# Performance work log

Measured on AMD Instinct MI355X. Metric: run time of the kernel, lower is better.

The kernel has to match this reference:

```python
import jax, jax.numpy as jnp
import numpy as np

V, H, B, T, L = 10000, 1024, 64, 32, 2  # vocab, hidden, batch, target_len, num_layers


def setup_inputs() -> dict:
    key = jax.random.key(0)
    ks = jax.random.split(key, 14)
    s = 1.0 / np.sqrt(H)  # PyTorch LSTM/Linear uniform init bound

    def u(k, shape):
        return jax.random.uniform(k, shape, jnp.float32, -s, s)

    return {
        "hidden": jax.random.normal(ks[0], (L, B, H), jnp.float32),
        "cell": jax.random.normal(ks[1], (L, B, H), jnp.float32),
        "captions": jax.random.randint(ks[2], (B, T), 0, V),
        "tf_mask": jax.random.randint(ks[3], (T,), 0, 2).astype(bool),
        # LSTM layer 0 (input = one-hot, size V)
        "W_ih_l0": u(ks[4], (4 * H, V)),
        "W_hh_l0": u(ks[5], (4 * H, H)),
        "b_ih_l0": u(ks[6], (4 * H,)),
        "b_hh_l0": u(ks[7], (4 * H,)),
        # LSTM layer 1
        "W_ih_l1": u(ks[8], (4 * H, H)),
        "W_hh_l1": u(ks[9], (4 * H, H)),
        "b_ih_l1": u(ks[10], (4 * H,)),
        "b_hh_l1": u(ks[11], (4 * H,)),
        # reverse_linear: hidden -> vocab
        "W_out": u(ks[12], (V, H)),
        "b_out": u(ks[13], (V,)),
    }


def _lstm_cell(x, h, c, Wih, Whh, bih, bhh):
    # PyTorch gate order: i, f, g, o
    gates = x @ Wih.T + h @ Whh.T + bih + bhh  # [B, 4H]
    i, f, g, o = jnp.split(gates, 4, axis=-1)
    c_new = jax.nn.sigmoid(f) * c + jax.nn.sigmoid(i) * jnp.tanh(g)
    h_new = jax.nn.sigmoid(o) * jnp.tanh(c_new)
    return h_new, c_new


def reference(hidden, cell, captions, tf_mask,
              W_ih_l0, W_hh_l0, b_ih_l0, b_hh_l0,
              W_ih_l1, W_hh_l1, b_ih_l1, b_hh_l1,
              W_out, b_out):
    inp0 = jax.nn.one_hot(captions[:, 0], V, dtype=jnp.float32)  # [B, V]
    carry = (hidden[0], cell[0], hidden[1], cell[1], inp0)

    def step(carry, xs):
        h1, c1, h2, c2, x = carry
        cap_t, tf_t = xs
        h1, c1 = _lstm_cell(x, h1, c1, W_ih_l0, W_hh_l0, b_ih_l0, b_hh_l0)
        h2, c2 = _lstm_cell(h1, h2, c2, W_ih_l1, W_hh_l1, b_ih_l1, b_hh_l1)
        logits = h2 @ W_out.T + b_out  # [B, V]
        nxt = jnp.where(tf_t, cap_t, jnp.argmax(logits, axis=-1))
        x = jax.nn.one_hot(nxt, V, dtype=jnp.float32)
        return (h1, c1, h2, c2, x), logits

    _, logits = jax.lax.scan(step, carry, (captions[:, 1:].T, tf_mask[1:]))  # [T-1, B, V]
    outputs = jnp.concatenate(
        [inp0[:, None, :], jnp.transpose(logits, (1, 0, 2))], axis=1)  # [B, T, V]
    return outputs
```

## Files before the change

### kernel.cpp

```cpp
#include <hip/hip_runtime.h>


#define HDIM 1024
#define BDIM 64
#define VDIM 10000
#define VPAD 10048
#define TDIM 32

typedef _Float16 f16;
typedef _Float16 f16x8 __attribute__((ext_vector_type(8)));
typedef float f32x4 __attribute__((ext_vector_type(4)));

#define WS_C1    0
#define WS_C2    262144
#define WS_H1H   524288
#define WS_H1L   655360
#define WS_H2H   786432
#define WS_H2L   917504
#define WS_CAND  1048576
#define WS_PRE0  1130496
#define WS_PRE1  5324800
#define WS_WB    13713408
#define SQB      8388608
#define WVO      20578304

__device__ __forceinline__ float sigmoidf_(float x) {
    return 1.0f / (1.0f + expf(-x));
}

__global__ __launch_bounds__(256) void gemm_as(
    const f16* __restrict__ Ah0, const f16* __restrict__ Al0,
    const f16* __restrict__ Wh0,
    const f16* __restrict__ Ah1, const f16* __restrict__ Al1,
    const f16* __restrict__ Wh1,
    float* __restrict__ part, int KS)
{
    const int tid = threadIdx.x;
    const int wave = tid >> 6, lane = tid & 63;
    const int wr = wave >> 1, wc = wave & 1;
    const int q = blockIdx.y, z = blockIdx.z;
    const f16* __restrict__ Ah = z ? Ah1 : Ah0;
    const f16* __restrict__ Al = z ? Al1 : Al0;
    const f16* __restrict__ Wh = z ? Wh1 : Wh0;
    const int klen = HDIM / KS;
    const int kbase = q * klen;
    const int n0 = blockIdx.x * 64 + wc * 32;
    const int m0 = wr * 32;
    const int lm = lane & 15, quad = lane >> 4;
    const int slab = z * KS + q;

    f32x4 acc[2][2] = {};
    f32x4 accL[2][2] = {};

    const f16* a_h = Ah + (size_t)(m0 + lm) * HDIM + kbase + quad * 8;
    const f16* a_l = Al + (size_t)(m0 + lm) * HDIM + kbase + quad * 8;
    const f16* b_h = Wh + (size_t)(n0 + lm) * HDIM + kbase + quad * 8;

    #pragma unroll 4
    for (int ko = 0; ko < klen; ko += 32) {
        f16x8 ah0 = *(const f16x8*)(a_h + ko);
        f16x8 ah1 = *(const f16x8*)(a_h + 16 * HDIM + ko);
        f16x8 al0 = *(const f16x8*)(a_l + ko);
        f16x8 al1 = *(const f16x8*)(a_l + 16 * HDIM + ko);
        f16x8 bh0 = *(const f16x8*)(b_h + ko);
        f16x8 bh1 = *(const f16x8*)(b_h + 16 * HDIM + ko);

        acc[0][0] = __builtin_amdgcn_mfma_f32_16x16x32_f16(ah0, bh0, acc[0][0], 0, 0, 0);
        acc[0][1] = __builtin_amdgcn_mfma_f32_16x16x32_f16(ah0, bh1, acc[0][1], 0, 0, 0);
        acc[1][0] = __builtin_amdgcn_mfma_f32_16x16x32_f16(ah1, bh0, acc[1][0], 0, 0, 0);
        acc[1][1] = __builtin_amdgcn_mfma_f32_16x16x32_f16(ah1, bh1, acc[1][1], 0, 0, 0);

        accL[0][0] = __builtin_amdgcn_mfma_f32_16x16x32_f16(al0, bh0, accL[0][0], 0, 0, 0);
        accL[0][1] = __builtin_amdgcn_mfma_f32_16x16x32_f16(al0, bh1, accL[0][1], 0, 0, 0);
        accL[1][0] = __builtin_amdgcn_mfma_f32_16x16x32_f16(al1, bh0, accL[1][0], 0, 0, 0);
        accL[1][1] = __builtin_amdgcn_mfma_f32_16x16x32_f16(al1, bh1, accL[1][1], 0, 0, 0);
    }

    float* dst = part + (size_t)slab * 262144;
    #pragma unroll
    for (int rt = 0; rt < 2; rt++)
        #pragma unroll
        for (int ct = 0; ct < 2; ct++)
            #pragma unroll
            for (int r = 0; r < 4; r++) {
                int row = m0 + rt * 16 + quad * 4 + r;
                int col = n0 + ct * 16 + lm;
                dst[(size_t)row * 4096 + col] =
                    acc[rt][ct][r] + accL[rt][ct][r] * (1.0f / 2048.0f);
            }
}

__global__ __launch_bounds__(256) void gemm_out_l0(
    const f16* __restrict__ h2h, const f16* __restrict__ h2l,
    const f16* __restrict__ Wouth, const f16* __restrict__ Woutl,
    const float* __restrict__ bout, float* __restrict__ out,
    unsigned long long* __restrict__ cand, int t,
    const f16* __restrict__ h1h, const f16* __restrict__ h1l,
    const f16* __restrict__ Whh0h, float* __restrict__ pre0)
{
    const int tid = threadIdx.x;
    const int wave = tid >> 6, lane = tid & 63;
    const int wr = wave >> 1, wc = wave & 1;
    const int lm = lane & 15, quad = lane >> 4;
    const int bx = blockIdx.x;

    if (bx < 157) {
        const int n0 = bx * 64 + wc * 32;
        const int m0 = wr * 32;
        f32x4 acc[2][2] = {};
        f32x4 accL[2][2] = {};
        const f16* a_h = h2h + (size_t)(m0 + lm) * HDIM + quad * 8;
        const f16* a_l = h2l + (size_t)(m0 + lm) * HDIM + quad * 8;
        const f16* b_h = Wouth + (size_t)(n0 + lm) * HDIM + quad * 8;
        const f16* b_l = Woutl + (size_t)(n0 + lm) * HDIM + quad * 8;

        #pragma unroll 4
        for (int ko = 0; ko < HDIM; ko += 32) {
            f16x8 ah0 = *(const f16x8*)(a_h + ko);
            f16x8 ah1 = *(const f16x8*)(a_h + 16 * HDIM + ko);
            f16x8 al0 = *(const f16x8*)(a_l + ko);
            f16x8 al1 = *(const f16x8*)(a_l + 16 * HDIM + ko);
            f16x8 bh0 = *(const f16x8*)(b_h + ko);
            f16x8 bh1 = *(const f16x8*)(b_h + 16 * HDIM + ko);
            f16x8 bl0 = *(const f16x8*)(b_l + ko);
            f16x8 bl1 = *(const f16x8*)(b_l + 16 * HDIM + ko);

            acc[0][0] = __builtin_amdgcn_mfma_f32_16x16x32_f16(ah0, bh0, acc[0][0], 0, 0, 0);
            acc[0][1] = __builtin_amdgcn_mfma_f32_16x16x32_f16(ah0, bh1, acc[0][1], 0, 0, 0);
            acc[1][0] = __builtin_amdgcn_mfma_f32_16x16x32_f16(ah1, bh0, acc[1][0], 0, 0, 0);
            acc[1][1] = __builtin_amdgcn_mfma_f32_16x16x32_f16(ah1, bh1, acc[1][1], 0, 0, 0);

            accL[0][0] = __builtin_amdgcn_mfma_f32_16x16x32_f16(ah0, bl0, accL[0][0], 0, 0, 0);
            accL[0][1] = __builtin_amdgcn_mfma_f32_16x16x32_f16(ah0, bl1, accL[0][1], 0, 0, 0);
            accL[1][0] = __builtin_amdgcn_mfma_f32_16x16x32_f16(ah1, bl0, accL[1][0], 0, 0, 0);
            accL[1][1] = __builtin_amdgcn_mfma_f32_16x16x32_f16(ah1, bl1, accL[1][1], 0, 0, 0);

            accL[0][0] = __builtin_amdgcn_mfma_f32_16x16x32_f16(al0, bh0, accL[0][0], 0, 0, 0);
            accL[0][1] = __builtin_amdgcn_mfma_f32_16x16x32_f16(al0, bh1, accL[0][1], 0, 0, 0);
            accL[1][0] = __builtin_amdgcn_mfma_f32_16x16x32_f16(al1, bh0, accL[1][0], 0, 0, 0);
            accL[1][1] = __builtin_amdgcn_mfma_f32_16x16x32_f16(al1, bh1, accL[1][1], 0, 0, 0);
        }

        __shared__ unsigned long long cs[64][2];
        float bo[2];
        #pragma unroll
        for (int ct = 0; ct < 2; ct++) {
            int col = n0 + ct * 16 + lm;
            bo[ct] = (col < VDIM) ? bout[col] : 0.0f;
        }
        #pragma unroll
        for (int rt = 0; rt < 2; rt++)
            #pragma unroll
            for (int r = 0; r < 4; r++) {
                int row = m0 + rt * 16 + quad * 4 + r;
                unsigned long long e = 0ull;
                #pragma unroll
                for (int ct = 0; ct < 2; ct++) {
                    int col = n0 + ct * 16 + lm;
                    if (col < VDIM) {
                        float s = acc[rt][ct][r] + accL[rt][ct][r] * (1.0f / 2048.0f)
                                + bo[ct];
                        out[(size_t)row * (TDIM * VDIM) + (size_t)t * VDIM + col] = s;
                        unsigned u = __float_as_uint(s);
                        u = (u & 0x80000000u) ? ~u : (u | 0x80000000u);
                        unsigned long long p =
                            ((unsigned long long)u << 32) | (unsigned)(~col);
                        if (p > e) e = p;
                    }
                }
                #pragma unroll
                for (int m = 1; m < 16; m <<= 1) {
                    unsigned long long o = __shfl_xor(e, m, 64);
                    if (o > e) e = o;
                }
                if (lm == 0) cs[row][wc] = e;
            }
        __syncthreads();
        if (tid < 64) {
            unsigned long long e = cs[tid][0];
            if (cs[tid][1] > e) e = cs[tid][1];
            cand[(size_t)tid * 157 + bx] = e;
        }
    } else {
        const int u = bx - 157;
        const int q = u >> 6;
        const int nt = u & 63;
        const int n0 = nt * 64 + wc * 32;
        const int m0 = wr * 32;
        const int kbase = q * 256;
        f32x4 acc[2][2] = {};
        f32x4 accL[2][2] = {};
        const f16* a_h = h1h + (size_t)(m0 + lm) * HDIM + kbase + quad * 8;
        const f16* a_l = h1l + (size_t)(m0 + lm) * HDIM + kbase + quad * 8;
        const f16* b_h = Whh0h + (size_t)(n0 + lm) * HDIM + kbase + quad * 8;

        #pragma unroll 4
        for (int ko = 0; ko < 256; ko += 32) {
            f16x8 ah0 = *(const f16x8*)(a_h + ko);
            f16x8 ah1 = *(const f16x8*)(a_h + 16 * HDIM + ko);
            f16x8 al0 = *(const f16x8*)(a_l + ko);
            f16x8 al1 = *(const f16x8*)(a_l + 16 * HDIM + ko);
            f16x8 bh0 = *(const f16x8*)(b_h + ko);
            f16x8 bh1 = *(const f16x8*)(b_h + 16 * HDIM + ko);

            acc[0][0] = __builtin_amdgcn_mfma_f32_16x16x32_f16(ah0, bh0, acc[0][0], 0, 0, 0);
            acc[0][1] = __builtin_amdgcn_mfma_f32_16x16x32_f16(ah0, bh1, acc[0][1], 0, 0, 0);
            acc[1][0] = __builtin_amdgcn_mfma_f32_16x16x32_f16(ah1, bh0, acc[1][0], 0, 0, 0);
            acc[1][1] = __builtin_amdgcn_mfma_f32_16x16x32_f16(ah1, bh1, acc[1][1], 0, 0, 0);

            accL[0][0] = __builtin_amdgcn_mfma_f32_16x16x32_f16(al0, bh0, accL[0][0], 0, 0, 0);
            accL[0][1] = __builtin_amdgcn_mfma_f32_16x16x32_f16(al0, bh1, accL[0][1], 0, 0, 0);
            accL[1][0] = __builtin_amdgcn_mfma_f32_16x16x32_f16(al1, bh0, accL[1][0], 0, 0, 0);
            accL[1][1] = __builtin_amdgcn_mfma_f32_16x16x32_f16(al1, bh1, accL[1][1], 0, 0, 0);
        }

        float* dst = pre0 + (size_t)q * 262144;
        #pragma unroll
        for (int rt = 0; rt < 2; rt++)
            #pragma unroll
            for (int ct = 0; ct < 2; ct++)
                #pragma unroll
                for (int r = 0; r < 4; r++) {
                    int row = m0 + rt * 16 + quad * 4 + r;
                    int col = n0 + ct * 16 + lm;
                    dst[(size_t)row * 4096 + col] =
                        acc[rt][ct][r] + accL[rt][ct][r] * (1.0f / 2048.0f);
                }
    }
}

__global__ __launch_bounds__(256) void convert_split(
    const float* __restrict__ src, f16* __restrict__ hi, f16* __restrict__ lo,
    int n_src, int n_pad)
{
    int i = blockIdx.x * 256 + threadIdx.x;
    if (i >= n_pad) return;
    float x = (i < n_src) ? src[i] : 0.0f;
    f16 h = (f16)x;
    hi[i] = h;
    if (lo) lo[i] = (f16)((x - (float)h) * 2048.0f);
}

__global__ __launch_bounds__(256) void cell0_kernel(
    const float* __restrict__ part,
    const float* __restrict__ Wih0, const float* __restrict__ bih,
    const float* __restrict__ bhh,
    const int* __restrict__ captions, const int* __restrict__ tfmask,
    const unsigned long long* __restrict__ cand,
    float* __restrict__ c1, f16* __restrict__ h1h, f16* __restrict__ h1l, int t)
{
    int tid = threadIdx.x;
    int idx = blockIdx.x * 256 + tid;
    int b = idx >> 10, i = idx & 1023;
    int tok;
    if (t == 1) {
        tok = captions[b * TDIM];
    } else if (tfmask[t - 1]) {
        tok = captions[b * TDIM + (t - 1)];
    } else {
        __shared__ unsigned long long red[4];
        __shared__ int tok_s;
        unsigned long long e = (tid < 157) ? cand[(size_t)b * 157 + tid] : 0ull;
        #pragma unroll
        for (int m = 32; m > 0; m >>= 1) {
            unsigned long long o = __shfl_down(e, m, 64);
            if (o > e) e = o;
        }
        if ((tid & 63) == 0) red[tid >> 6] = e;
        __syncthreads();
        if (tid == 0) {
            e = red[0];
            if (red[1] > e) e = red[1];
            if (red[2] > e) e = red[2];
            if (red[3] > e) e = red[3];
            tok_s = (int)(~(unsigned)(e & 0xffffffffull));
        }
        __syncthreads();
        tok = tok_s;
    }

    float g[4];
    #pragma unroll
    for (int gi = 0; gi < 4; gi++) {
        int j = gi * HDIM + i;
        float s = bih[j] + bhh[j] + Wih0[(size_t)j * VDIM + tok];
        #pragma unroll
        for (int q = 0; q < 4; q++) s += part[(size_t)q * 262144 + b * 4096 + j];
        g[gi] = s;
    }
    float ig = sigmoidf_(g[0]), fg = sigmoidf_(g[1]);
    float gg = tanhf(g[2]),     og = sigmoidf_(g[3]);
    float cn = fg * c1[idx] + ig * gg;
    float hn = og * tanhf(cn);
    c1[idx] = cn;
    f16 hh = (f16)hn;
    h1h[idx] = hh;
    h1l[idx] = (f16)((hn - (float)hh) * 2048.0f);
}

__global__ __launch_bounds__(256) void cell1_kernel(
    const float* __restrict__ part,
    const float* __restrict__ bih, const float* __restrict__ bhh,
    float* __restrict__ c2, f16* __restrict__ h2h, f16* __restrict__ h2l)
{
    int idx = blockIdx.x * 256 + threadIdx.x;
    int b = idx >> 10, i = idx & 1023;
    float g[4];
    #pragma unroll
    for (int gi = 0; gi < 4; gi++) {
        int j = gi * HDIM + i;
        float s = bih[j] + bhh[j];
        #pragma unroll
        for (int q = 0; q < 8; q++) s += part[(size_t)q * 262144 + b * 4096 + j];
        g[gi] = s;
    }
    float ig = sigmoidf_(g[0]), fg = sigmoidf_(g[1]);
    float gg = tanhf(g[2]),     og = sigmoidf_(g[3]);
    float cn = fg * c2[idx] + ig * gg;
    float hn = og * tanhf(cn);
    c2[idx] = cn;
    f16 hh = (f16)hn;
    h2h[idx] = hh;
    h2l[idx] = (f16)((hn - (float)hh) * 2048.0f);
}

__global__ __launch_bounds__(256) void init_kernel(
    const float* __restrict__ hidden, const float* __restrict__ cell,
    const int* __restrict__ captions,
    float* __restrict__ c1, float* __restrict__ c2,
    f16* __restrict__ h1h, f16* __restrict__ h1l,
    f16* __restrict__ h2h, f16* __restrict__ h2l,
    float* __restrict__ out)
{
    int idx = blockIdx.x * 256 + threadIdx.x;
    if (idx < BDIM * HDIM) {
        float a = hidden[idx];
        float b = hidden[BDIM * HDIM + idx];
        c1[idx] = cell[idx];
        c2[idx] = cell[BDIM * HDIM + idx];
        f16 ah = (f16)a;
        h1h[idx] = ah; h1l[idx] = (f16)((a - (float)ah) * 2048.0f);
        f16 bh = (f16)b;
        h2h[idx] = bh; h2l[idx] = (f16)((b - (float)bh) * 2048.0f);
    }
    if (idx < BDIM * VDIM) {
        int b = idx / VDIM, v = idx % VDIM;
        out[(size_t)b * TDIM * VDIM + v] = (v == captions[b * TDIM]) ? 1.0f : 0.0f;
    }
}

extern "C" void kernel_launch(void* const* d_in, const int* in_sizes, int n_in,
                              void* d_out, int out_size, void* d_ws, size_t ws_size,
                              hipStream_t stream)
{
    const float* hidden   = (const float*)d_in[0];
    const float* cellin   = (const float*)d_in[1];
    const int*   captions = (const int*)d_in[2];
    const int*   tfmask   = (const int*)d_in[3];
    const float* Wih0 = (const float*)d_in[4];
    const float* Whh0 = (const float*)d_in[5];
    const float* bih0 = (const float*)d_in[6];
    const float* bhh0 = (const float*)d_in[7];
    const float* Wih1 = (const float*)d_in[8];
    const float* Whh1 = (const float*)d_in[9];
    const float* bih1 = (const float*)d_in[10];
    const float* bhh1 = (const float*)d_in[11];
    const float* Wout = (const float*)d_in[12];
    const float* bout = (const float*)d_in[13];
    float* out = (float*)d_out;

    char* wsb = (char*)d_ws;
    float* c1 = (float*)(wsb + WS_C1);
    float* c2 = (float*)(wsb + WS_C2);
    f16* h1h = (f16*)(wsb + WS_H1H);
    f16* h1l = (f16*)(wsb + WS_H1L);
    f16* h2h = (f16*)(wsb + WS_H2H);
    f16* h2l = (f16*)(wsb + WS_H2L);
    unsigned long long* cand = (unsigned long long*)(wsb + WS_CAND);
    float* pre0 = (float*)(wsb + WS_PRE0);
    float* pre1 = (float*)(wsb + WS_PRE1);
    f16* Whh0h = (f16*)(wsb + WS_WB);
    f16* Wih1h = (f16*)(wsb + WS_WB + 1 * (size_t)SQB);
    f16* Whh1h = (f16*)(wsb + WS_WB + 2 * (size_t)SQB);
    f16* Wouth = (f16*)(wsb + WS_WB + 3 * (size_t)SQB);
    f16* Woutl = (f16*)(wsb + WS_WB + 3 * (size_t)SQB + (size_t)WVO);

    init_kernel<<<2500, 256, 0, stream>>>(hidden, cellin, captions,
                                          c1, c2, h1h, h1l, h2h, h2l, out);
    int nsq = 4096 * 1024;
    convert_split<<<nsq / 256, 256, 0, stream>>>(Whh0, Whh0h, (f16*)0, nsq, nsq);
    convert_split<<<nsq / 256, 256, 0, stream>>>(Wih1, Wih1h, (f16*)0, nsq, nsq);
    convert_split<<<nsq / 256, 256, 0, stream>>>(Whh1, Whh1h, (f16*)0, nsq, nsq);
    int nvo = VPAD * 1024;
    convert_split<<<nvo / 256, 256, 0, stream>>>(Wout, Wouth, Woutl,
                                                 VDIM * 1024, nvo);

    gemm_as<<<dim3(64, 4, 1), 256, 0, stream>>>(
        h1h, h1l, Whh0h, h1h, h1l, Whh0h, pre0, 4);

    for (int t = 1; t < TDIM; t++) {
        cell0_kernel<<<256, 256, 0, stream>>>(pre0, Wih0, bih0, bhh0,
                                              captions, tfmask, cand,
                                              c1, h1h, h1l, t);
        gemm_as<<<dim3(64, 4, 2), 256, 0, stream>>>(
            h1h, h1l, Wih1h, h2h, h2l, Whh1h, pre1, 4);
        cell1_kernel<<<256, 256, 0, stream>>>(pre1, bih1, bhh1, c2, h2h, h2l);
        int nb = (t < TDIM - 1) ? 413 : 157;
        gemm_out_l0<<<nb, 256, 0, stream>>>(h2h, h2l, Wouth, Woutl, bout,
                                            out, cand, t,
                                            h1h, h1l, Whh0h, pre0);
    }
}
```

Baseline: 2.335 ms.

## Swizzle output weights into MFMA fragment layout and halve split-K partitions

Output projection weights are pre-swizzled into a per-lane MFMA fragment order so each wave loads contiguous 16-byte chunks. Each block now covers 64 vocab columns with two K-halves reduced through shared memory, and every wave handles all 64 batch rows. Split-K for the recurrent GEMMs drops from 4 to 2 slices, which cuts partial-sum traffic and cell-kernel reads but gives fewer blocks. The argmax candidate array is widened to 314 tiles per row and is reduced in cell0.

```diff
diff --git a/kernel.cpp b/kernel.cpp
--- a/kernel.cpp
+++ b/kernel.cpp
@@ -5,6 +5,7 @@
 #define BDIM 64
 #define VDIM 10000
 #define VPAD 10048
+#define NTOUT 314
 #define TDIM 32
 
 typedef _Float16 f16;
@@ -18,9 +19,9 @@
 #define WS_H2H   786432
 #define WS_H2L   917504
 #define WS_CAND  1048576
-#define WS_PRE0  1130496
-#define WS_PRE1  5324800
-#define WS_WB    13713408
+#define WS_PRE0  1212416
+#define WS_PRE1  3309568
+#define WS_WB    7503872
 #define SQB      8388608
 #define WVO      20578304
 
@@ -92,102 +93,112 @@
 
 __global__ __launch_bounds__(256) void gemm_out_l0(
     const f16* __restrict__ h2h, const f16* __restrict__ h2l,
-    const f16* __restrict__ Wouth, const f16* __restrict__ Woutl,
+    const f16* __restrict__ Wsh, const f16* __restrict__ Wsl,
     const float* __restrict__ bout, float* __restrict__ out,
     unsigned long long* __restrict__ cand, int t,
     const f16* __restrict__ h1h, const f16* __restrict__ h1l,
     const f16* __restrict__ Whh0h, float* __restrict__ pre0)
 {
-    const int tid = threadIdx.x;
+    const int tid = threadIdx.x, bx = blockIdx.x;
     const int wave = tid >> 6, lane = tid & 63;
-    const int wr = wave >> 1, wc = wave & 1;
     const int lm = lane & 15, quad = lane >> 4;
-    const int bx = blockIdx.x;
 
     if (bx < 157) {
-        const int n0 = bx * 64 + wc * 32;
-        const int m0 = wr * 32;
-        f32x4 acc[2][2] = {};
-        f32x4 accL[2][2] = {};
-        const f16* a_h = h2h + (size_t)(m0 + lm) * HDIM + quad * 8;
-        const f16* a_l = h2l + (size_t)(m0 + lm) * HDIM + quad * 8;
-        const f16* b_h = Wouth + (size_t)(n0 + lm) * HDIM + quad * 8;
-        const f16* b_l = Woutl + (size_t)(n0 + lm) * HDIM + quad * 8;
+        const int tl = wave & 1;
+        const int kh = wave >> 1;
+        const int gt = bx * 2 + tl;
+        f32x4 acc[4][2] = {};
+        f32x4 accL[4][2] = {};
+        const f16* a_h = h2h + (size_t)lm * HDIM + kh * 512 + quad * 8;
+        const f16* a_l = h2l + (size_t)lm * HDIM + kh * 512 + quad * 8;
+        const f16* w_h = Wsh + (size_t)gt * 32768 + (size_t)kh * 16384 + lane * 8;
+        const f16* w_l = Wsl + (size_t)gt * 32768 + (size_t)kh * 16384 + lane * 8;
 
         #pragma unroll 4
-        for (int ko = 0; ko < HDIM; ko += 32) {
-            f16x8 ah0 = *(const f16x8*)(a_h + ko);
-            f16x8 ah1 = *(const f16x8*)(a_h + 16 * HDIM + ko);
-            f16x8 al0 = *(const f16x8*)(a_l + ko);
-            f16x8 al1 = *(const f16x8*)(a_l + 16 * HDIM + ko);
-            f16x8 bh0 = *(const f16x8*)(b_h + ko);
-            f16x8 bh1 = *(const f16x8*)(b_h + 16 * HDIM + ko);
-            f16x8 bl0 = *(const f16x8*)(b_l + ko);
-            f16x8 bl1 = *(const f16x8*)(b_l + 16 * HDIM + ko);
-
-            acc[0][0] = __builtin_amdgcn_mfma_f32_16x16x32_f16(ah0, bh0, acc[0][0], 0, 0, 0);
-            acc[0][1] = __builtin_amdgcn_mfma_f32_16x16x32_f16(ah0, bh1, acc[0][1], 0, 0, 0);
-            acc[1][0] = __builtin_amdgcn_mfma_f32_16x16x32_f16(ah1, bh0, acc[1][0], 0, 0, 0);
-            acc[1][1] = __builtin_amdgcn_mfma_f32_16x16x32_f16(ah1, bh1, acc[1][1], 0, 0, 0);
-
-            accL[0][0] = __builtin_amdgcn_mfma_f32_16x16x32_f16(ah0, bl0, accL[0][0], 0, 0, 0);
-            accL[0][1] = __builtin_amdgcn_mfma_f32_16x16x32_f16(ah0, bl1, accL[0][1], 0, 0, 0);
-            accL[1][0] = __builtin_amdgcn_mfma_f32_16x16x32_f16(ah1, bl0, accL[1][0], 0, 0, 0);
-            accL[1][1] = __builtin_amdgcn_mfma_f32_16x16x32_f16(ah1, bl1, accL[1][1], 0, 0, 0);
-
-            accL[0][0] = __builtin_amdgcn_mfma_f32_16x16x32_f16(al0, bh0, accL[0][0], 0, 0, 0);
-            accL[0][1] = __builtin_amdgcn_mfma_f32_16x16x32_f16(al0, bh1, accL[0][1], 0, 0, 0);
-            accL[1][0] = __builtin_amdgcn_mfma_f32_16x16x32_f16(al1, bh0, accL[1][0], 0, 0, 0);
-            accL[1][1] = __builtin_amdgcn_mfma_f32_16x16x32_f16(al1, bh1, accL[1][1], 0, 0, 0);
-        }
-
-        __shared__ unsigned long long cs[64][2];
-        float bo[2];
-        #pragma unroll
-        for (int ct = 0; ct < 2; ct++) {
-            int col = n0 + ct * 16 + lm;
-            bo[ct] = (col < VDIM) ? bout[col] : 0.0f;
-        }
-        #pragma unroll
-        for (int rt = 0; rt < 2; rt++)
-            #pragma unroll
-            for (int r = 0; r < 4; r++) {
-                int row = m0 + rt * 16 + quad * 4 + r;
-                unsigned long long e = 0ull;
+        for (int kb = 0; kb < 16; kb++) {
+            f16x8 bh0 = *(const f16x8*)(w_h + kb * 1024);
+            f16x8 bh1 = *(const f16x8*)(w_h + kb * 1024 + 512);
+            f16x8 bl0 = *(const f16x8*)(w_l + kb * 1024);
+            f16x8 bl1 = *(const f16x8*)(w_l + kb * 1024 + 512);
+            f16x8 ah[4], al[4];
+            #pragma unroll
+            for (int mt = 0; mt < 4; mt++) {
+                ah[mt] = *(const f16x8*)(a_h + mt * (16 * HDIM) + kb * 32);
+                al[mt] = *(const f16x8*)(a_l + mt * (16 * HDIM) + kb * 32);
+            }
+            #pragma unroll
+            for (int mt = 0; mt < 4; mt++) {
+                acc[mt][0]  = __builtin_amdgcn_mfma_f32_16x16x32_f16(ah[mt], bh0, acc[mt][0], 0, 0, 0);
+                acc[mt][1]  = __builtin_amdgcn_mfma_f32_16x16x32_f16(ah[mt], bh1, acc[mt][1], 0, 0, 0);
+                accL[mt][0] = __builtin_amdgcn_mfma_f32_16x16x32_f16(al[mt], bh0, accL[mt][0], 0, 0, 0);
+                accL[mt][1] = __builtin_amdgcn_mfma_f32_16x16x32_f16(al[mt], bh1, accL[mt][1], 0, 0, 0);
+                accL[mt][0] = __builtin_amdgcn_mfma_f32_16x16x32_f16(ah[mt], bl0, accL[mt][0], 0, 0, 0);
+                accL[mt][1] = __builtin_amdgcn_mfma_f32_16x16x32_f16(ah[mt], bl1, accL[mt][1], 0, 0, 0);
+            }
+        }
+
+        float part_[4][2][4];
+        #pragma unroll
+        for (int mt = 0; mt < 4; mt++)
+            #pragma unroll
+            for (int c = 0; c < 2; c++)
                 #pragma unroll
-                for (int ct = 0; ct < 2; ct++) {
-                    int col = n0 + ct * 16 + lm;
-                    if (col < VDIM) {
-                        float s = acc[rt][ct][r] + accL[rt][ct][r] * (1.0f / 2048.0f)
-                                + bo[ct];
-                        out[(size_t)row * (TDIM * VDIM) + (size_t)t * VDIM + col] = s;
-                        unsigned u = __float_as_uint(s);
-                        u = (u & 0x80000000u) ? ~u : (u | 0x80000000u);
-                        unsigned long long p =
-                            ((unsigned long long)u << 32) | (unsigned)(~col);
-                        if (p > e) e = p;
+                for (int r = 0; r < 4; r++)
+                    part_[mt][c][r] = acc[mt][c][r] + accL[mt][c][r] * (1.0f / 2048.0f);
+
+        __shared__ float lds[2][64][33];
+        if (kh == 1) {
+            #pragma unroll
+            for (int mt = 0; mt < 4; mt++)
+                #pragma unroll
+                for (int c = 0; c < 2; c++)
+                    #pragma unroll
+                    for (int r = 0; r < 4; r++)
+                        lds[tl][mt * 16 + quad * 4 + r][c * 16 + lm] = part_[mt][c][r];
+        }
+        __syncthreads();
+        if (kh == 0) {
+            float bo[2];
+            #pragma unroll
+            for (int c = 0; c < 2; c++) {
+                int col = gt * 32 + c * 16 + lm;
+                bo[c] = (col < VDIM) ? bout[col] : 0.0f;
+            }
+            #pragma unroll
+            for (int mt = 0; mt < 4; mt++)
+                #pragma unroll
+                for (int r = 0; r < 4; r++) {
+                    int row = mt * 16 + quad * 4 + r;
+                    unsigned long long e = 0ull;
+                    #pragma unroll
+                    for (int c = 0; c < 2; c++) {
+                        int col = gt * 32 + c * 16 + lm;
+                        float sv = part_[mt][c][r] + lds[tl][row][c * 16 + lm] + bo[c];
+                        if (col < VDIM) {
+                            out[(size_t)row * (TDIM * VDIM) + (size_t)t * VDIM + col] = sv;
+                            unsigned u = __float_as_uint(sv);
+                            u = (u & 0x80000000u) ? ~u : (u | 0x80000000u);
+                            unsigned long long p =
+                                ((unsigned long long)u << 32) | (unsigned)(~col);
+                            if (p > e) e = p;
+                        }
                     }
+                    #pragma unroll
+                    for (int m = 1; m < 16; m <<= 1) {
+                        unsigned long long o = __shfl_xor(e, m, 64);
+                        if (o > e) e = o;
+                    }
+                    if (lm == 0) cand[(size_t)row * NTOUT + gt] = e;
                 }
-                #pragma unroll
-                for (int m = 1; m < 16; m <<= 1) {
-                    unsigned long long o = __shfl_xor(e, m, 64);
-                    if (o > e) e = o;
-                }
-                if (lm == 0) cs[row][wc] = e;
-            }
-        __syncthreads();
-        if (tid < 64) {
-            unsigned long long e = cs[tid][0];
-            if (cs[tid][1] > e) e = cs[tid][1];
-            cand[(size_t)tid * 157 + bx] = e;
         }
     } else {
+        const int wr = wave >> 1, wc = wave & 1;
         const int u = bx - 157;
         const int q = u >> 6;
         const int nt = u & 63;
         const int n0 = nt * 64 + wc * 32;
         const int m0 = wr * 32;
-        const int kbase = q * 256;
+        const int kbase = q * 512;
         f32x4 acc[2][2] = {};
         f32x4 accL[2][2] = {};
         const f16* a_h = h1h + (size_t)(m0 + lm) * HDIM + kbase + quad * 8;
@@ -195,7 +206,7 @@
         const f16* b_h = Whh0h + (size_t)(n0 + lm) * HDIM + kbase + quad * 8;
 
         #pragma unroll 4
-        for (int ko = 0; ko < 256; ko += 32) {
+        for (int ko = 0; ko < 512; ko += 32) {
             f16x8 ah0 = *(const f16x8*)(a_h + ko);
             f16x8 ah1 = *(const f16x8*)(a_h + 16 * HDIM + ko);
             f16x8 al0 = *(const f16x8*)(a_l + ko);
@@ -229,16 +240,38 @@
     }
 }
 
-__global__ __launch_bounds__(256) void convert_split(
-    const float* __restrict__ src, f16* __restrict__ hi, f16* __restrict__ lo,
-    int n_src, int n_pad)
+__global__ __launch_bounds__(256) void convert_hi(
+    const float* __restrict__ src, f16* __restrict__ hi, int n)
 {
     int i = blockIdx.x * 256 + threadIdx.x;
-    if (i >= n_pad) return;
-    float x = (i < n_src) ? src[i] : 0.0f;
-    f16 h = (f16)x;
-    hi[i] = h;
-    if (lo) lo[i] = (f16)((x - (float)h) * 2048.0f);
+    if (i >= n) return;
+    hi[i] = (f16)src[i];
+}
+
+__global__ __launch_bounds__(256) void conv_swz_out(
+    const float* __restrict__ src, f16* __restrict__ hi, f16* __restrict__ lo)
+{
+    int o = blockIdx.x * 256 + threadIdx.x;
+    if (o >= NTOUT * 4096) return;
+    int lane = o & 63, c = (o >> 6) & 1, kb = (o >> 7) & 31, nt = o >> 12;
+    int row = nt * 32 + c * 16 + (lane & 15);
+    int col = kb * 32 + ((lane >> 4) << 3);
+    float f[8] = {};
+    if (row < VDIM) {
+        float4 v0 = *(const float4*)(src + (size_t)row * HDIM + col);
+        float4 v1 = *(const float4*)(src + (size_t)row * HDIM + col + 4);
+        f[0] = v0.x; f[1] = v0.y; f[2] = v0.z; f[3] = v0.w;
+        f[4] = v1.x; f[5] = v1.y; f[6] = v1.z; f[7] = v1.w;
+    }
+    f16x8 H, L;
+    #pragma unroll
+    for (int e = 0; e < 8; e++) {
+        f16 h = (f16)f[e];
+        H[e] = h;
+        L[e] = (f16)((f[e] - (float)h) * 2048.0f);
+    }
+    *(f16x8*)(hi + (size_t)o * 8) = H;
+    *(f16x8*)(lo + (size_t)o * 8) = L;
 }
 
 __global__ __launch_bounds__(256) void cell0_kernel(
@@ -260,7 +293,12 @@
     } else {
         __shared__ unsigned long long red[4];
         __shared__ int tok_s;
-        unsigned long long e = (tid < 157) ? cand[(size_t)b * 157 + tid] : 0ull;
+        unsigned long long e = 0ull;
+        if (tid < 157) {
+            e = cand[(size_t)b * NTOUT + tid];
+            unsigned long long e2 = cand[(size_t)b * NTOUT + 157 + tid];
+            if (e2 > e) e = e2;
+        }
         #pragma unroll
         for (int m = 32; m > 0; m >>= 1) {
             unsigned long long o = __shfl_down(e, m, 64);
@@ -285,7 +323,7 @@
         int j = gi * HDIM + i;
         float s = bih[j] + bhh[j] + Wih0[(size_t)j * VDIM + tok];
         #pragma unroll
-        for (int q = 0; q < 4; q++) s += part[(size_t)q * 262144 + b * 4096 + j];
+        for (int q = 0; q < 2; q++) s += part[(size_t)q * 262144 + b * 4096 + j];
         g[gi] = s;
     }
     float ig = sigmoidf_(g[0]), fg = sigmoidf_(g[1]);
@@ -311,7 +349,7 @@
         int j = gi * HDIM + i;
         float s = bih[j] + bhh[j];
         #pragma unroll
-        for (int q = 0; q < 8; q++) s += part[(size_t)q * 262144 + b * 4096 + j];
+        for (int q = 0; q < 4; q++) s += part[(size_t)q * 262144 + b * 4096 + j];
         g[gi] = s;
     }
     float ig = sigmoidf_(g[0]), fg = sigmoidf_(g[1]);
@@ -388,24 +426,22 @@
     init_kernel<<<2500, 256, 0, stream>>>(hidden, cellin, captions,
                                           c1, c2, h1h, h1l, h2h, h2l, out);
     int nsq = 4096 * 1024;
-    convert_split<<<nsq / 256, 256, 0, stream>>>(Whh0, Whh0h, (f16*)0, nsq, nsq);
-    convert_split<<<nsq / 256, 256, 0, stream>>>(Wih1, Wih1h, (f16*)0, nsq, nsq);
-    convert_split<<<nsq / 256, 256, 0, stream>>>(Whh1, Whh1h, (f16*)0, nsq, nsq);
-    int nvo = VPAD * 1024;
-    convert_split<<<nvo / 256, 256, 0, stream>>>(Wout, Wouth, Woutl,
-                                                 VDIM * 1024, nvo);
-
-    gemm_as<<<dim3(64, 4, 1), 256, 0, stream>>>(
-        h1h, h1l, Whh0h, h1h, h1l, Whh0h, pre0, 4);
+    convert_hi<<<nsq / 256, 256, 0, stream>>>(Whh0, Whh0h, nsq);
+    convert_hi<<<nsq / 256, 256, 0, stream>>>(Wih1, Wih1h, nsq);
+    convert_hi<<<nsq / 256, 256, 0, stream>>>(Whh1, Whh1h, nsq);
+    conv_swz_out<<<(NTOUT * 4096 + 255) / 256, 256, 0, stream>>>(Wout, Wouth, Woutl);
+
+    gemm_as<<<dim3(64, 2, 1), 256, 0, stream>>>(
+        h1h, h1l, Whh0h, h1h, h1l, Whh0h, pre0, 2);
 
     for (int t = 1; t < TDIM; t++) {
         cell0_kernel<<<256, 256, 0, stream>>>(pre0, Wih0, bih0, bhh0,
                                               captions, tfmask, cand,
                                               c1, h1h, h1l, t);
-        gemm_as<<<dim3(64, 4, 2), 256, 0, stream>>>(
-            h1h, h1l, Wih1h, h2h, h2l, Whh1h, pre1, 4);
+        gemm_as<<<dim3(64, 2, 2), 256, 0, stream>>>(
+            h1h, h1l, Wih1h, h2h, h2l, Whh1h, pre1, 2);
         cell1_kernel<<<256, 256, 0, stream>>>(pre1, bih1, bhh1, c2, h2h, h2l);
-        int nb = (t < TDIM - 1) ? 413 : 157;
+        int nb = (t < TDIM - 1) ? 285 : 157;
         gemm_out_l0<<<nb, 256, 0, stream>>>(h2h, h2l, Wouth, Woutl, bout,
                                             out, cand, t,
                                             h1h, h1l, Whh0h, pre0);
```

Measured after the change: 2.189 ms. -6.3%, faster.
